# Optimization experiments

Hardware: AMD Instinct MI355X
Metric: run time of the kernel (lower is better)

The kernel has to match this reference:

```python
import jax, jax.numpy as jnp
import numpy as np

DIM = 1024
HEADS = 16
HEAD_DIM = DIM // HEADS


def setup_inputs() -> dict:
    key = jax.random.key(0)
    k_x, k_qkv, k_ow, k_ob = jax.random.split(key, 4)
    x = jax.random.normal(k_x, (2, 2048, DIM), dtype=jnp.float32)
    # nn.Linear(dim, 3*dim, bias=False): weight shape [3*dim, dim], y = x @ W.T
    w_qkv = jax.random.normal(k_qkv, (3 * DIM, DIM), dtype=jnp.float32) * (DIM ** -0.5)
    # nn.Linear(dim, dim) with bias
    w_o = jax.random.normal(k_ow, (DIM, DIM), dtype=jnp.float32) * (DIM ** -0.5)
    b_o = jax.random.normal(k_ob, (DIM,), dtype=jnp.float32) * 0.02
    return {"x": x, "w_qkv": w_qkv, "w_o": w_o, "b_o": b_o}


def reference(x, w_qkv, w_o, b_o):
    b, n, _ = x.shape
    scale = DIM ** -0.5  # NOTE: source scales by full dim, not head dim
    # qkv projection: [b, n, 3*dim]
    qkv = jnp.einsum('bnd,ed->bne', x, w_qkv)
    # 'b n (qkv h d) -> qkv b h n d'
    qkv = qkv.reshape(b, n, 3, HEADS, HEAD_DIM)
    q = jnp.transpose(qkv[:, :, 0], (0, 2, 1, 3))  # [b, h, n, d]
    k = jnp.transpose(qkv[:, :, 1], (0, 2, 1, 3))
    v = jnp.transpose(qkv[:, :, 2], (0, 2, 1, 3))
    scores = jnp.einsum('bhqd,bhkd->bhqk', q, k) * scale  # [b, h, n, n]
    attn = jax.nn.softmax(scores, axis=-1)
    out = jnp.einsum('bhqk,bhkd->bhqd', attn, v)  # [b, h, n, d]
    out = jnp.transpose(out, (0, 2, 1, 3)).reshape(b, n, DIM)  # 'b h n d -> b n (h d)'
    out = jnp.einsum('bnd,ed->bne', out, w_o) + b_o
    return out
```

## Files before the change

kernel.cpp:

```cpp
#include <hip/hip_runtime.h>
#include <stdint.h>


#define DIM 1024
#define SEQ 2048
#define BATCH 2
#define ROWS 4096
#define RSTRIDE 3072

typedef __bf16 bf16_t;
typedef bf16_t bf16x4 __attribute__((ext_vector_type(4)));
typedef bf16_t bf16x8 __attribute__((ext_vector_type(8)));
typedef float f32x4 __attribute__((ext_vector_type(4)));

__device__ __forceinline__ ushort f2bf(float f) {
    uint32_t u;
    __builtin_memcpy(&u, &f, 4);
    uint32_t r = (u + 0x7fffu + ((u >> 16) & 1u)) >> 16;
    return (ushort)r;
}

__device__ __forceinline__ void store_out(ushort* p, float v) { *p = f2bf(v); }
__device__ __forceinline__ void store_out(float* p, float v) { *p = v; }

__device__ __forceinline__ void gl_lds16(const void* g, void* l) {
    __builtin_amdgcn_global_load_lds(
        (const __attribute__((address_space(1))) void*)g,
        (__attribute__((address_space(3))) void*)l, 16, 0, 0);
}

__global__ __launch_bounds__(256) void cvt3_kernel(
    const float* __restrict__ x, const float* __restrict__ wq,
    const float* __restrict__ wo, ushort* __restrict__ dst) {
    size_t i = ((size_t)blockIdx.x * 256 + threadIdx.x) * 8;
    const size_t n_x = (size_t)ROWS * DIM;
    const size_t n_wq = (size_t)3 * DIM * DIM;
    const float* src;
    size_t off;
    if (i < n_x) {
        src = x; off = i;
    } else if (i < n_x + n_wq) {
        src = wq; off = i - n_x;
    } else {
        src = wo; off = i - n_x - n_wq;
    }
    float4 a = *(const float4*)(src + off);
    float4 b = *(const float4*)(src + off + 4);
    uint4 u;
    u.x = (uint)f2bf(a.x) | ((uint)f2bf(a.y) << 16);
    u.y = (uint)f2bf(a.z) | ((uint)f2bf(a.w) << 16);
    u.z = (uint)f2bf(b.x) | ((uint)f2bf(b.y) << 16);
    u.w = (uint)f2bf(b.z) | ((uint)f2bf(b.w) << 16);
    *(uint4*)(dst + i) = u;
}

template <typename OutT>
__global__ __launch_bounds__(256) void gemm_bt_kernel(
    const ushort* __restrict__ A, const ushort* __restrict__ B,
    const float* __restrict__ bias, OutT* __restrict__ C,
    int M, int N, int K) {
    __shared__ __align__(16) ushort sA[128 * 64];
    __shared__ __align__(16) ushort sB[128 * 64];

    const int tid = threadIdx.x;
    const int lane = tid & 63, w = tid >> 6;
    const int quad = lane >> 4, l15 = lane & 15;
    const int wm = (w >> 1) * 64, wn = (w & 1) * 64;
    const int bm = blockIdx.y, bn = blockIdx.x;

    f32x4 acc[4][4];
#pragma unroll
    for (int i = 0; i < 4; i++)
#pragma unroll
        for (int j = 0; j < 4; j++) acc[i][j] = (f32x4){0.f, 0.f, 0.f, 0.f};

    const ushort* Abase = A + (size_t)(bm * 128) * K;
    const ushort* Bbase = B + (size_t)(bn * 128) * K;
    const int rd = lane >> 3, c8 = lane & 7;
    const int sw = l15 & 7;

    for (int kk = 0; kk < K; kk += 64) {
        __syncthreads();
#pragma unroll
        for (int t = 0; t < 4; t++) {
            int row = w * 32 + t * 8;
            gl_lds16(Abase + (size_t)(row + rd) * K + kk + ((c8 ^ rd) * 8),
                     sA + row * 64);
            gl_lds16(Bbase + (size_t)(row + rd) * K + kk + ((c8 ^ rd) * 8),
                     sB + row * 64);
        }
        __syncthreads();

#pragma unroll
        for (int kh = 0; kh < 2; kh++) {
            bf16x8 af[4], bfr[4];
#pragma unroll
            for (int i = 0; i < 4; i++)
                af[i] = *(const bf16x8*)((const bf16_t*)sA +
                        (wm + i * 16 + l15) * 64 + (((kh * 4 + quad) ^ sw) * 8));
#pragma unroll
            for (int j = 0; j < 4; j++)
                bfr[j] = *(const bf16x8*)((const bf16_t*)sB +
                        (wn + j * 16 + l15) * 64 + (((kh * 4 + quad) ^ sw) * 8));
#pragma unroll
            for (int i = 0; i < 4; i++)
#pragma unroll
                for (int j = 0; j < 4; j++)
                    acc[i][j] = __builtin_amdgcn_mfma_f32_16x16x32_bf16(
                        af[i], bfr[j], acc[i][j], 0, 0, 0);
        }
    }

#pragma unroll
    for (int i = 0; i < 4; i++)
#pragma unroll
        for (int j = 0; j < 4; j++) {
            int col = bn * 128 + wn + j * 16 + l15;
            float bv = bias ? bias[col] : 0.f;
#pragma unroll
            for (int r = 0; r < 4; r++) {
                int row = bm * 128 + wm + i * 16 + quad * 4 + r;
                store_out(&C[(size_t)row * N + col], acc[i][j][r] + bv);
            }
        }
}

__global__ __launch_bounds__(512) void flash_attn_kernel(
    const ushort* __restrict__ qkv, ushort* __restrict__ out) {
    __shared__ __align__(16) ushort sK[128 * 64];
    __shared__ __align__(16) ushort sVt[64 * 128];
    __shared__ __align__(16) ushort sP[128 * 64];

    const int tid = threadIdx.x;
    const int lane = tid & 63, w = tid >> 6;
    const int quad = lane >> 4, l15 = lane & 15;
    const int sw = l15 & 7;
    const int bh = blockIdx.y, b = bh >> 4, h = bh & 15;
    const int q0 = blockIdx.x * 128;
    const ushort* qkvb = qkv + (size_t)b * SEQ * RSTRIDE + h * 64;

    const ushort* qrow = qkvb + (size_t)(q0 + w * 16 + l15) * RSTRIDE;
    const bf16x8 aq0 = *(const bf16x8*)(qrow + quad * 8);
    const bf16x8 aq1 = *(const bf16x8*)(qrow + 32 + quad * 8);

    const int krow = tid >> 3, kc8 = tid & 7;
    const int kdst = krow * 64 + ((kc8 ^ (krow & 7)) * 8);
    const int vrp = tid & 63, vc = tid >> 6;
    const int vch = vrp >> 2, vlo = vrp & 3;

    uint4 kreg0, kreg1, va, vb;
    {
        const ushort* kp0 = qkvb + (size_t)krow * RSTRIDE + DIM + kc8 * 8;
        kreg0 = *(const uint4*)kp0;
        kreg1 = *(const uint4*)(kp0 + (size_t)64 * RSTRIDE);
        const ushort* v0 = qkvb + (size_t)(2 * vrp) * RSTRIDE + 2 * DIM + vc * 8;
        va = *(const uint4*)v0;
        vb = *(const uint4*)(v0 + RSTRIDE);
    }

    f32x4 l_acc = (f32x4){0.f, 0.f, 0.f, 0.f};
    f32x4 o[4];
#pragma unroll
    for (int j = 0; j < 4; j++) o[j] = (f32x4){0.f, 0.f, 0.f, 0.f};

    bf16x8 vones;
#pragma unroll
    for (int e = 0; e < 8; e++) vones[e] = (bf16_t)1.0f;

    const float c_exp = 0.04508422f;

    uint* vt32 = (uint*)sVt;
    bf16_t* sPb = (bf16_t*)sP;

    *(uint4*)(sK + kdst) = kreg0;
    *(uint4*)(sK + 64 * 64 + kdst) = kreg1;
    __syncthreads();

    for (int kb = 0; kb < SEQ; kb += 128) {
        {
            int base = (vc * 8) * 64 + vlo;
            vt32[base + 0 * 64 + ((vch ^ 0) << 2)] = (va.x & 0xffffu) | (vb.x << 16);
            vt32[base + 1 * 64 + ((vch ^ 1) << 2)] = (va.x >> 16) | (vb.x & 0xffff0000u);
            vt32[base + 2 * 64 + ((vch ^ 2) << 2)] = (va.y & 0xffffu) | (vb.y << 16);
            vt32[base + 3 * 64 + ((vch ^ 3) << 2)] = (va.y >> 16) | (vb.y & 0xffff0000u);
            vt32[base + 4 * 64 + ((vch ^ 4) << 2)] = (va.z & 0xffffu) | (vb.z << 16);
            vt32[base + 5 * 64 + ((vch ^ 5) << 2)] = (va.z >> 16) | (vb.z & 0xffff0000u);
            vt32[base + 6 * 64 + ((vch ^ 6) << 2)] = (va.w & 0xffffu) | (vb.w << 16);
            vt32[base + 7 * 64 + ((vch ^ 7) << 2)] = (va.w >> 16) | (vb.w & 0xffff0000u);
        }

        f32x4 s[8];
#pragma unroll
        for (int j = 0; j < 8; j++) {
            const ushort* kp = sK + (j * 16 + l15) * 64;
            bf16x8 bk0 = *(const bf16x8*)(kp + ((quad ^ sw) * 8));
            bf16x8 bk1 = *(const bf16x8*)(kp + (((4 | quad) ^ sw) * 8));
            f32x4 z = (f32x4){0.f, 0.f, 0.f, 0.f};
            __builtin_amdgcn_s_setprio(1);
            z = __builtin_amdgcn_mfma_f32_16x16x32_bf16(aq0, bk0, z, 0, 0, 0);
            z = __builtin_amdgcn_mfma_f32_16x16x32_bf16(aq1, bk1, z, 0, 0, 0);
            __builtin_amdgcn_s_setprio(0);
            s[j] = z;
        }

        int nkb = (kb + 128 < SEQ) ? kb + 128 : kb;
        {
            const ushort* kp0 = qkvb + (size_t)(nkb + krow) * RSTRIDE + DIM + kc8 * 8;
            kreg0 = *(const uint4*)kp0;
            kreg1 = *(const uint4*)(kp0 + (size_t)64 * RSTRIDE);
            const ushort* v0 =
                qkvb + (size_t)(nkb + 2 * vrp) * RSTRIDE + 2 * DIM + vc * 8;
            va = *(const uint4*)v0;
            vb = *(const uint4*)(v0 + RSTRIDE);
        }
        __syncthreads();

#pragma unroll
        for (int h2 = 0; h2 < 2; h2++) {
#pragma unroll
            for (int j = 0; j < 4; j++)
#pragma unroll
                for (int r = 0; r < 4; r++) {
                    float p = __builtin_amdgcn_exp2f(s[h2 * 4 + j][r] * c_exp);
                    int row = w * 16 + quad * 4 + r;
                    int ch = j * 2 + (l15 >> 3);
                    sPb[row * 64 +
                        (((ch ^ ((quad * 4 + r) & 7)) << 3) | (l15 & 7))] =
                        (bf16_t)p;
                }
            const bf16_t* pp = sPb + (w * 16 + l15) * 64;
            bf16x8 pa0 = *(const bf16x8*)(pp + ((quad ^ sw) * 8));
            bf16x8 pa1 = *(const bf16x8*)(pp + (((4 | quad) ^ sw) * 8));
            __builtin_amdgcn_s_setprio(1);
            l_acc = __builtin_amdgcn_mfma_f32_16x16x32_bf16(pa0, vones, l_acc, 0, 0, 0);
            l_acc = __builtin_amdgcn_mfma_f32_16x16x32_bf16(pa1, vones, l_acc, 0, 0, 0);
            __builtin_amdgcn_s_setprio(0);
#pragma unroll
            for (int jd = 0; jd < 4; jd++) {
                const bf16_t* vp = (const bf16_t*)sVt + (jd * 16 + l15) * 128;
                bf16x8 bv0 = *(const bf16x8*)(vp + (((h2 * 8 + quad) ^ sw) * 8));
                bf16x8 bv1 = *(const bf16x8*)(vp + (((h2 * 8 + 4 + quad) ^ sw) * 8));
                __builtin_amdgcn_s_setprio(1);
                o[jd] = __builtin_amdgcn_mfma_f32_16x16x32_bf16(pa0, bv0, o[jd], 0, 0, 0);
                o[jd] = __builtin_amdgcn_mfma_f32_16x16x32_bf16(pa1, bv1, o[jd], 0, 0, 0);
                __builtin_amdgcn_s_setprio(0);
            }
        }

        *(uint4*)(sK + kdst) = kreg0;
        *(uint4*)(sK + 64 * 64 + kdst) = kreg1;
        __syncthreads();
    }

#pragma unroll
    for (int r = 0; r < 4; r++) {
        float inv = 1.f / l_acc[r];
        int qrow_i = q0 + w * 16 + quad * 4 + r;
#pragma unroll
        for (int j = 0; j < 4; j++) {
            out[(size_t)(b * SEQ + qrow_i) * DIM + h * 64 + j * 16 + l15] =
                f2bf(o[j][r] * inv);
        }
    }
}

extern "C" void kernel_launch(void* const* d_in, const int* in_sizes, int n_in,
                              void* d_out, int out_size, void* d_ws, size_t ws_size,
                              hipStream_t stream) {
    const float* x = (const float*)d_in[0];
    const float* w_qkv = (const float*)d_in[1];
    const float* w_o = (const float*)d_in[2];
    const float* b_o = (const float*)d_in[3];
    float* out = (float*)d_out;

    ushort* qkv = (ushort*)d_ws;
    ushort* attn = qkv + (size_t)ROWS * 3 * DIM;
    ushort* xb = attn + (size_t)ROWS * DIM;
    ushort* wqkvb = xb + (size_t)ROWS * DIM;
    ushort* wob = wqkvb + (size_t)3 * DIM * DIM;

    dim3 blk(256);
    cvt3_kernel<<<(ROWS * DIM + 3 * DIM * DIM + DIM * DIM) / 2048, blk, 0,
                  stream>>>(x, w_qkv, w_o, xb);

    gemm_bt_kernel<ushort><<<dim3(3 * DIM / 128, ROWS / 128), blk, 0, stream>>>(
        xb, wqkvb, nullptr, qkv, ROWS, 3 * DIM, DIM);
    flash_attn_kernel<<<dim3(SEQ / 128, BATCH * 16), dim3(512), 0, stream>>>(qkv, attn);
    gemm_bt_kernel<float><<<dim3(DIM / 128, ROWS / 128), blk, 0, stream>>>(
        attn, wob, b_o, out, ROWS, DIM, DIM);
}
```

Baseline: 202.7 us.

## Restructure attention loop prefetch/sync, fix P swizzle, narrow output GEMM tile

The flash attention loop now writes the prefetched K and V tiles to shared memory at the top of each iteration, then issues the next global loads right after the barrier so they overlap the QK and PV MFMA work. This reduces the loop to a different pair of barriers. The P-tile LDS swizzle gets an extra XOR term to cut bank conflicts on the P writes and reads. The GEMM is templated on its N tile width, and the output projection uses a 64-wide tile, giving twice as many blocks for better CU occupancy at the cost of less operand reuse per block.

New measurement: 191.9 us. 5.4% less time.

```diff
diff --git a/kernel.cpp b/kernel.cpp
--- a/kernel.cpp
+++ b/kernel.cpp
@@ -54,28 +54,29 @@
     *(uint4*)(dst + i) = u;
 }
 
-template <typename OutT>
+template <typename OutT, int BN>
 __global__ __launch_bounds__(256) void gemm_bt_kernel(
     const ushort* __restrict__ A, const ushort* __restrict__ B,
     const float* __restrict__ bias, OutT* __restrict__ C,
     int M, int N, int K) {
+    constexpr int JN = BN / 32;
     __shared__ __align__(16) ushort sA[128 * 64];
-    __shared__ __align__(16) ushort sB[128 * 64];
+    __shared__ __align__(16) ushort sB[BN * 64];
 
     const int tid = threadIdx.x;
     const int lane = tid & 63, w = tid >> 6;
     const int quad = lane >> 4, l15 = lane & 15;
-    const int wm = (w >> 1) * 64, wn = (w & 1) * 64;
+    const int wm = (w >> 1) * 64, wn = (w & 1) * (BN / 2);
     const int bm = blockIdx.y, bn = blockIdx.x;
 
-    f32x4 acc[4][4];
+    f32x4 acc[4][JN];
 #pragma unroll
     for (int i = 0; i < 4; i++)
 #pragma unroll
-        for (int j = 0; j < 4; j++) acc[i][j] = (f32x4){0.f, 0.f, 0.f, 0.f};
+        for (int j = 0; j < JN; j++) acc[i][j] = (f32x4){0.f, 0.f, 0.f, 0.f};
 
     const ushort* Abase = A + (size_t)(bm * 128) * K;
-    const ushort* Bbase = B + (size_t)(bn * 128) * K;
+    const ushort* Bbase = B + (size_t)(bn * BN) * K;
     const int rd = lane >> 3, c8 = lane & 7;
     const int sw = l15 & 7;
 
@@ -86,6 +87,10 @@
             int row = w * 32 + t * 8;
             gl_lds16(Abase + (size_t)(row + rd) * K + kk + ((c8 ^ rd) * 8),
                      sA + row * 64);
+        }
+#pragma unroll
+        for (int t = 0; t < BN / 32; t++) {
+            int row = w * 8 + t * 32;
             gl_lds16(Bbase + (size_t)(row + rd) * K + kk + ((c8 ^ rd) * 8),
                      sB + row * 64);
         }
@@ -93,19 +98,19 @@
 
 #pragma unroll
         for (int kh = 0; kh < 2; kh++) {
-            bf16x8 af[4], bfr[4];
+            bf16x8 af[4], bfr[JN];
 #pragma unroll
             for (int i = 0; i < 4; i++)
                 af[i] = *(const bf16x8*)((const bf16_t*)sA +
                         (wm + i * 16 + l15) * 64 + (((kh * 4 + quad) ^ sw) * 8));
 #pragma unroll
-            for (int j = 0; j < 4; j++)
+            for (int j = 0; j < JN; j++)
                 bfr[j] = *(const bf16x8*)((const bf16_t*)sB +
                         (wn + j * 16 + l15) * 64 + (((kh * 4 + quad) ^ sw) * 8));
 #pragma unroll
             for (int i = 0; i < 4; i++)
 #pragma unroll
-                for (int j = 0; j < 4; j++)
+                for (int j = 0; j < JN; j++)
                     acc[i][j] = __builtin_amdgcn_mfma_f32_16x16x32_bf16(
                         af[i], bfr[j], acc[i][j], 0, 0, 0);
         }
@@ -114,8 +119,8 @@
 #pragma unroll
     for (int i = 0; i < 4; i++)
 #pragma unroll
-        for (int j = 0; j < 4; j++) {
-            int col = bn * 128 + wn + j * 16 + l15;
+        for (int j = 0; j < JN; j++) {
+            int col = bn * BN + wn + j * 16 + l15;
             float bv = bias ? bias[col] : 0.f;
 #pragma unroll
             for (int r = 0; r < 4; r++) {
@@ -171,12 +176,10 @@
 
     uint* vt32 = (uint*)sVt;
     bf16_t* sPb = (bf16_t*)sP;
-
-    *(uint4*)(sK + kdst) = kreg0;
-    *(uint4*)(sK + 64 * 64 + kdst) = kreg1;
-    __syncthreads();
-
+    const int swp = (l15 & 7) ^ (((l15 >> 3) & 1) << 1);
     for (int kb = 0; kb < SEQ; kb += 128) {
+        *(uint4*)(sK + kdst) = kreg0;
+        *(uint4*)(sK + 64 * 64 + kdst) = kreg1;
         {
             int base = (vc * 8) * 64 + vlo;
             vt32[base + 0 * 64 + ((vch ^ 0) << 2)] = (va.x & 0xffffu) | (vb.x << 16);
@@ -188,6 +191,18 @@
             vt32[base + 6 * 64 + ((vch ^ 6) << 2)] = (va.w & 0xffffu) | (vb.w << 16);
             vt32[base + 7 * 64 + ((vch ^ 7) << 2)] = (va.w >> 16) | (vb.w & 0xffff0000u);
         }
+        __syncthreads();
+
+        int nkb = (kb + 128 < SEQ) ? kb + 128 : kb;
+        {
+            const ushort* kp0 = qkvb + (size_t)(nkb + krow) * RSTRIDE + DIM + kc8 * 8;
+            kreg0 = *(const uint4*)kp0;
+            kreg1 = *(const uint4*)(kp0 + (size_t)64 * RSTRIDE);
+            const ushort* v0 =
+                qkvb + (size_t)(nkb + 2 * vrp) * RSTRIDE + 2 * DIM + vc * 8;
+            va = *(const uint4*)v0;
+            vb = *(const uint4*)(v0 + RSTRIDE);
+        }
 
         f32x4 s[8];
 #pragma unroll
@@ -203,18 +218,6 @@
             s[j] = z;
         }
 
-        int nkb = (kb + 128 < SEQ) ? kb + 128 : kb;
-        {
-            const ushort* kp0 = qkvb + (size_t)(nkb + krow) * RSTRIDE + DIM + kc8 * 8;
-            kreg0 = *(const uint4*)kp0;
-            kreg1 = *(const uint4*)(kp0 + (size_t)64 * RSTRIDE);
-            const ushort* v0 =
-                qkvb + (size_t)(nkb + 2 * vrp) * RSTRIDE + 2 * DIM + vc * 8;
-            va = *(const uint4*)v0;
-            vb = *(const uint4*)(v0 + RSTRIDE);
-        }
-        __syncthreads();
-
 #pragma unroll
         for (int h2 = 0; h2 < 2; h2++) {
 #pragma unroll
@@ -222,15 +225,16 @@
 #pragma unroll
                 for (int r = 0; r < 4; r++) {
                     float p = __builtin_amdgcn_exp2f(s[h2 * 4 + j][r] * c_exp);
-                    int row = w * 16 + quad * 4 + r;
+                    int kr = quad * 4 + r;
+                    int row = w * 16 + kr;
                     int ch = j * 2 + (l15 >> 3);
-                    sPb[row * 64 +
-                        (((ch ^ ((quad * 4 + r) & 7)) << 3) | (l15 & 7))] =
+                    int key = (kr & 7) ^ (((kr >> 3) & 1) << 1);
+                    sPb[row * 64 + (((ch ^ key) << 3) | (l15 & 7))] =
                         (bf16_t)p;
                 }
             const bf16_t* pp = sPb + (w * 16 + l15) * 64;
-            bf16x8 pa0 = *(const bf16x8*)(pp + ((quad ^ sw) * 8));
-            bf16x8 pa1 = *(const bf16x8*)(pp + (((4 | quad) ^ sw) * 8));
+            bf16x8 pa0 = *(const bf16x8*)(pp + ((quad ^ swp) * 8));
+            bf16x8 pa1 = *(const bf16x8*)(pp + (((4 | quad) ^ swp) * 8));
             __builtin_amdgcn_s_setprio(1);
             l_acc = __builtin_amdgcn_mfma_f32_16x16x32_bf16(pa0, vones, l_acc, 0, 0, 0);
             l_acc = __builtin_amdgcn_mfma_f32_16x16x32_bf16(pa1, vones, l_acc, 0, 0, 0);
@@ -246,9 +250,6 @@
                 __builtin_amdgcn_s_setprio(0);
             }
         }
-
-        *(uint4*)(sK + kdst) = kreg0;
-        *(uint4*)(sK + 64 * 64 + kdst) = kreg1;
         __syncthreads();
     }
 
@@ -283,9 +284,11 @@
     cvt3_kernel<<<(ROWS * DIM + 3 * DIM * DIM + DIM * DIM) / 2048, blk, 0,
                   stream>>>(x, w_qkv, w_o, xb);
 
-    gemm_bt_kernel<ushort><<<dim3(3 * DIM / 128, ROWS / 128), blk, 0, stream>>>(
-        xb, wqkvb, nullptr, qkv, ROWS, 3 * DIM, DIM);
+    gemm_bt_kernel<ushort, 128>
+        <<<dim3(3 * DIM / 128, ROWS / 128), blk, 0, stream>>>(
+            xb, wqkvb, nullptr, qkv, ROWS, 3 * DIM, DIM);
     flash_attn_kernel<<<dim3(SEQ / 128, BATCH * 16), dim3(512), 0, stream>>>(qkv, attn);
-    gemm_bt_kernel<float><<<dim3(DIM / 128, ROWS / 128), blk, 0, stream>>>(
-        attn, wob, b_o, out, ROWS, DIM, DIM);
-}
+    gemm_bt_kernel<float, 64>
+        <<<dim3(DIM / 64, ROWS / 128), blk, 0, stream>>>(
+            attn, wob, b_o, out, ROWS, DIM, DIM);
+}
```
